# Performance work log

Hardware: AMD Instinct MI355X
Metric: run time of the kernel (lower is better)

The kernel has to match this reference:

```python
import jax, jax.numpy as jnp
import numpy as np

ROPE_BASE = 1024.0
EPS = 1e-6

def _rms_norm(x):
    return x / jnp.sqrt(jnp.mean(x * x, axis=-1, keepdims=True) + EPS)

def _rotary_tables(T, head_dim):
    steps = head_dim // 4
    inv_freq = (1.0 / ROPE_BASE) ** jnp.linspace(0.0, 1.0, steps, dtype=jnp.float32)
    inv_freq = jnp.concatenate([inv_freq, jnp.zeros(steps, dtype=jnp.float32)])  # [head_dim//2]
    theta = jnp.arange(T, dtype=jnp.float32)[:, None] * inv_freq[None, :]  # [T, head_dim//2]
    return jnp.cos(theta), jnp.sin(theta)

def _apply_rotary(x, cos, sin):
    # x: [B,H,T,hd]; cos/sin: [T, hd//2]
    d = x.shape[-1] // 2
    x1, x2 = x[..., :d], x[..., d:]
    return jnp.concatenate([x1 * cos + x2 * sin, -x1 * sin + x2 * cos], axis=-1)

def setup_inputs() -> dict:
    key = jax.random.key(0)
    ks = jax.random.split(key, 5)
    B, T, C = 4, 2048, 1024
    return {
        "x": jax.random.normal(ks[0], (B, T, C), dtype=jnp.float32),
        "v1": jax.random.normal(ks[1], (B, T, C), dtype=jnp.float32),
        "qkv_weight": 0.02 * jax.random.normal(ks[2], (3, C, C), dtype=jnp.float32),
        "c_proj_w": 0.02 * jax.random.normal(ks[3], (C, C), dtype=jnp.float32),
        "c_proj_b": jnp.zeros((C,), dtype=jnp.float32),
        "lamb": jnp.full((1,), 0.5, dtype=jnp.float32),
        "attn_window": 512,
    }

def reference(x, v1, qkv_weight, c_proj_w, c_proj_b, lamb, attn_window):
    B, T, C = x.shape
    H = 16
    hd = C // H
    # fused QKV projection: qkv_weight is [3, C, C], applied as x @ W_k^T
    qkv = jnp.einsum('btc,kdc->kbtd', x, qkv_weight)  # [3,B,T,C]
    q, k, v = qkv[0], qkv[1], qkv[2]
    def to_heads(t):
        return t.reshape(B, T, H, hd).transpose(0, 2, 1, 3)  # [B,H,T,hd]
    query, key_, value = to_heads(q), to_heads(k), to_heads(v)
    v1h = to_heads(v1)
    lam = lamb[0]
    value = (1.0 - lam) * value + lam * v1h  # value-residual blend
    query = _rms_norm(query)
    key_ = _rms_norm(key_)
    cos, sin = _rotary_tables(T, hd)
    query = _apply_rotary(query, cos, sin)
    key_ = _apply_rotary(key_, cos, sin)
    # windowed causal mask: attend iff 0 <= i - j < attn_window
    i = jnp.arange(T)[:, None]
    j = jnp.arange(T)[None, :]
    allowed = (i - j < attn_window) & (j <= i)
    bias = jnp.where(allowed, 0.0, -jnp.inf).astype(x.dtype)  # [T,T]
    scale = 1.0 / jnp.sqrt(jnp.asarray(hd, dtype=x.dtype))
    scores = jnp.einsum('bhtd,bhsd->bhts', query, key_) * scale + bias
    attn = jax.nn.softmax(scores, axis=-1)
    out = jnp.einsum('bhts,bhsd->bhtd', attn, value)  # [B,H,T,hd]
    out = out.transpose(0, 2, 1, 3).reshape(B, T, C)
    y = out @ c_proj_w.T + c_proj_b
    return (y, value)
```

## Files before the change

### kernel.cpp

```cpp
#include <hip/hip_runtime.h>
#include <stdint.h>

typedef __attribute__((ext_vector_type(8))) short short8;
typedef __attribute__((ext_vector_type(4))) float f32x4;

#define LDS_AS __attribute__((address_space(3)))
#define GLOB_AS __attribute__((address_space(1)))

__device__ __forceinline__ void gload_lds16(const void* g, void* l) {
    __builtin_amdgcn_global_load_lds((const GLOB_AS uint32_t*)g,
                                     (LDS_AS uint32_t*)l, 16, 0, 0);
}

__device__ __forceinline__ unsigned short f2bf(float f) {
    uint32_t u = __builtin_bit_cast(uint32_t, f);
    u += 0x7fffu + ((u >> 16) & 1u);
    return (unsigned short)(u >> 16);
}
__device__ __forceinline__ float bf2f(unsigned short u) {
    uint32_t v = ((uint32_t)u) << 16;
    return __builtin_bit_cast(float, v);
}

__global__ void cvt3_kernel(const float* __restrict__ s0,
                            const float* __restrict__ s1,
                            const float* __restrict__ s2,
                            unsigned short* __restrict__ d0,
                            unsigned short* __restrict__ d1,
                            unsigned short* __restrict__ d2) {
    long e = ((long)blockIdx.x * blockDim.x + threadIdx.x) * 4;
    const float* s; unsigned short* d; long off;
    if (e < 8388608)        { s = s0; d = d0; off = e; }
    else if (e < 11534336)  { s = s1; d = d1; off = e - 8388608; }
    else                    { s = s2; d = d2; off = e - 11534336; }
    float4 v = *(const float4*)(s + off);
    ushort4 o;
    o.x = f2bf(v.x); o.y = f2bf(v.y); o.z = f2bf(v.z); o.w = f2bf(v.w);
    *(ushort4*)(d + off) = o;
}

__global__ void rope_tables(float* __restrict__ cosT, float* __restrict__ sinT) {
    int tid = blockIdx.x * blockDim.x + threadIdx.x;
    int t = tid >> 5, i = tid & 31;
    float f = (i < 16) ? exp2f(-10.0f * (float)i / 15.0f) : 0.0f;
    float th = (float)t * f;
    cosT[tid] = cosf(th);
    sinT[tid] = sinf(th);
}

template <int MODE>
__global__ __launch_bounds__(512, 2) void gemm8p(
    const unsigned short* __restrict__ A, const unsigned short* __restrict__ B,
    int K,
    unsigned short* __restrict__ qbuf, unsigned short* __restrict__ kbuf,
    float* __restrict__ vout, unsigned short* __restrict__ vbT,
    const float* __restrict__ v1, const float* __restrict__ lambp,
    float* __restrict__ y, const float* __restrict__ bias,
    const float* __restrict__ cosT, const float* __restrict__ sinT)
{
    __shared__ __align__(16) char smem[147456];
    char* const AL = smem;
    char* const BL = smem + 98304;
    const int tid = threadIdx.x, lane = tid & 63, w = tid >> 6;
    const int wr = w >> 1, wc = w & 1;
    const int lr = lane & 15, lh = lane >> 4;

    const int id = blockIdx.x;
    const long m0 = (long)((id & 7) * 4 + ((id >> 3) & 3)) * 256;
    const long n0 = (long)(id >> 5) * 128;
    const int NT = K >> 6;

    const int srow = tid >> 3;
    const int swc  = (tid & 7) ^ (srow & 7);
    const long rsb = (long)K * 2;
    const char* pa0 = (const char*)A + (m0 + srow +   0) * rsb + swc * 16;
    const char* pa1 = (const char*)A + (m0 + srow +  64) * rsb + swc * 16;
    const char* pa2 = (const char*)A + (m0 + srow + 128) * rsb + swc * 16;
    const char* pa3 = (const char*)A + (m0 + srow + 192) * rsb + swc * 16;
    const char* pb0 = (const char*)B + (n0 + srow +   0) * rsb + swc * 16;
    const char* pb1 = (const char*)B + (n0 + srow +  64) * rsb + swc * 16;
    char* const lA = AL + w * 1024;
    char* const lB = BL + w * 1024;

    auto STAGE_A3 = [&](int aoff, int boff) {
        gload_lds16(pa0, lA + aoff);
        gload_lds16(pa1, lA + aoff + 8192);
        gload_lds16(pb0, lB + boff);
    };
    auto STAGE_B3 = [&](int aoff, int boff) {
        gload_lds16(pa2, lA + aoff + 16384);
        gload_lds16(pa3, lA + aoff + 24576);
        gload_lds16(pb1, lB + boff + 8192);
        pa0 += 128; pa1 += 128; pa2 += 128; pa3 += 128;
        pb0 += 128; pb1 += 128;
    };

    const int arow_b = (wr * 64 + lr) * 128;
    const int brow_b = (wc * 64 + lr) * 128;
    const int x0 = ((lh)     ^ (lr & 7)) * 16;
    const int x1 = ((4 + lh) ^ (lr & 7)) * 16;

    f32x4 acc[4][4] = {};

    STAGE_A3(0, 0);           STAGE_B3(0, 0);
    STAGE_A3(32768, 16384);   STAGE_B3(32768, 16384);

    int cA = 0, cB = 0;
    int sA = 65536, sB = 32768;

    for (int t = 0; t < NT; ++t) {
        if (t < NT - 1) asm volatile("s_waitcnt vmcnt(6)" ::: "memory");
        else            asm volatile("s_waitcnt vmcnt(0)" ::: "memory");
        __builtin_amdgcn_s_barrier();
        __builtin_amdgcn_sched_barrier(0);

        const char* ab = AL + cA;
        const char* bb = BL + cB;
        const bool st = (t < NT - 2);

        short8 bfr[4][2], afr[2][2];
        #pragma unroll
        for (int ni = 0; ni < 4; ++ni) {
            bfr[ni][0] = *(const short8*)(bb + brow_b + ni * 2048 + x0);
            bfr[ni][1] = *(const short8*)(bb + brow_b + ni * 2048 + x1);
        }
        #pragma unroll
        for (int mi = 0; mi < 2; ++mi) {
            afr[mi][0] = *(const short8*)(ab + arow_b + mi * 2048 + x0);
            afr[mi][1] = *(const short8*)(ab + arow_b + mi * 2048 + x1);
        }
        if (st) STAGE_A3(sA, sB);
        __builtin_amdgcn_s_barrier();
        asm volatile("s_waitcnt lgkmcnt(0)" ::: "memory");
        __builtin_amdgcn_sched_barrier(0);
        __builtin_amdgcn_s_setprio(1);
        #pragma unroll
        for (int mi = 0; mi < 2; ++mi)
            #pragma unroll
            for (int ni = 0; ni < 4; ++ni)
                #pragma unroll
                for (int ks = 0; ks < 2; ++ks)
                    acc[mi][ni] = __builtin_amdgcn_mfma_f32_16x16x32_bf16(
                        afr[mi][ks], bfr[ni][ks], acc[mi][ni], 0, 0, 0);
        __builtin_amdgcn_s_setprio(0);
        __builtin_amdgcn_s_barrier();

        short8 afr2[2][2];
        #pragma unroll
        for (int mi = 0; mi < 2; ++mi) {
            afr2[mi][0] = *(const short8*)(ab + arow_b + (mi + 2) * 2048 + x0);
            afr2[mi][1] = *(const short8*)(ab + arow_b + (mi + 2) * 2048 + x1);
        }
        if (st) STAGE_B3(sA, sB);
        __builtin_amdgcn_s_barrier();
        asm volatile("s_waitcnt lgkmcnt(0)" ::: "memory");
        __builtin_amdgcn_sched_barrier(0);
        __builtin_amdgcn_s_setprio(1);
        #pragma unroll
        for (int mi = 0; mi < 2; ++mi)
            #pragma unroll
            for (int ni = 0; ni < 4; ++ni)
                #pragma unroll
                for (int ks = 0; ks < 2; ++ks)
                    acc[mi + 2][ni] = __builtin_amdgcn_mfma_f32_16x16x32_bf16(
                        afr2[mi][ks], bfr[ni][ks], acc[mi + 2][ni], 0, 0, 0);
        __builtin_amdgcn_s_setprio(0);

        cA = (cA == 65536) ? 0 : cA + 32768;
        cB = (cB == 32768) ? 0 : cB + 16384;
        sA = (sA == 65536) ? 0 : sA + 32768;
        sB = (sB == 32768) ? 0 : sB + 16384;
    }

    if constexpr (MODE == 1) {
        const long nbase = n0 + wc * 64;
        const int kk = (int)(nbase >> 10);
        const int h = (int)((nbase & 1023) >> 6);
        if (kk == 2) {
            float lam = lambp[0];
            #pragma unroll
            for (int i = 0; i < 4; ++i)
            #pragma unroll
            for (int j = 0; j < 4; ++j)
            #pragma unroll
            for (int r = 0; r < 4; ++r) {
                long m = m0 + wr * 64 + i * 16 + lh * 4 + r;
                int d = j * 16 + lr;
                int rem = h * 64 + d;
                long b_ = m >> 11, t = m & 2047;
                size_t idx = (((size_t)(b_ * 16 + h)) * 2048 + t) * 64 + d;
                float vv = v1[(size_t)m * 1024 + rem];
                float val = (1.0f - lam) * acc[i][j][r] + lam * vv;
                vout[idx] = val;
                vbT[(((size_t)(b_ * 16 + h)) * 64 + d) * 2048 + t] = f2bf(val);
            }
        } else {
            unsigned short* dst = (kk == 0) ? qbuf : kbuf;
            #pragma unroll
            for (int i = 0; i < 4; ++i)
            #pragma unroll
            for (int r = 0; r < 4; ++r) {
                float v0 = acc[i][0][r], v1_ = acc[i][1][r];
                float v2 = acc[i][2][r], v3 = acc[i][3][r];
                float ss = v0 * v0 + v1_ * v1_ + v2 * v2 + v3 * v3;
                ss += __shfl_xor(ss, 1);
                ss += __shfl_xor(ss, 2);
                ss += __shfl_xor(ss, 4);
                ss += __shfl_xor(ss, 8);
                float inv = rsqrtf(ss * (1.0f / 64.0f) + 1e-6f);
                float x0f = v0 * inv, x1f = v1_ * inv;
                float x2f = v2 * inv, x3f = v3 * inv;
                long m = m0 + wr * 64 + i * 16 + lh * 4 + r;
                int t = (int)(m & 2047);
                long b_ = m >> 11;
                float c0 = cosT[t * 32 + lr],      s0 = sinT[t * 32 + lr];
                float c1 = cosT[t * 32 + 16 + lr], s1 = sinT[t * 32 + 16 + lr];
                size_t rb = (((size_t)(b_ * 16 + h)) * 2048 + t) * 64;
                dst[rb + 0 * 16 + lr] = f2bf( x0f * c0 + x2f * s0);
                dst[rb + 1 * 16 + lr] = f2bf( x1f * c1 + x3f * s1);
                dst[rb + 2 * 16 + lr] = f2bf(-x0f * s0 + x2f * c0);
                dst[rb + 3 * 16 + lr] = f2bf(-x1f * s1 + x3f * c1);
            }
        }
    } else {
        #pragma unroll
        for (int i = 0; i < 4; ++i)
        #pragma unroll
        for (int j = 0; j < 4; ++j)
        #pragma unroll
        for (int r = 0; r < 4; ++r) {
            long m = m0 + wr * 64 + i * 16 + lh * 4 + r;
            long n = n0 + wc * 64 + j * 16 + lr;
            y[(size_t)m * 1024 + n] = acc[i][j][r] + bias[n];
        }
    }
}

__global__ __launch_bounds__(512, 2) void attn_kernel(
    const unsigned short* __restrict__ qn, const unsigned short* __restrict__ kn,
    const unsigned short* __restrict__ vtb, unsigned short* __restrict__ attn_out,
    const int* __restrict__ winp)
{
    __shared__ unsigned short Ks[2][64 * 64];
    __shared__ unsigned short Vt[2][64 * 64];
    __shared__ unsigned short Pl[8][16 * 72];
    const int tid = threadIdx.x, lane = tid & 63, w = tid >> 6;
    const int lr = lane & 15, lh = lane >> 4;
    const int bh = blockIdx.x;
    const int qt2 = blockIdx.y;
    const int t0 = qt2 * 128;
    const int win = winp[0];
    const int qrow = t0 + w * 16;

    short8 qf[2];
    #pragma unroll
    for (int ks = 0; ks < 2; ++ks)
        qf[ks] = *(const short8*)&qn[((size_t)bh * 2048 + qrow + lr) * 64 + ks * 32 + lh * 8];

    const int srow = tid >> 3;
    const int scol = (tid & 7) ^ (srow & 7);
    const char* kg = (const char*)kn + ((size_t)bh * 2048 + srow) * 128 + scol * 16;
    const char* vg = (const char*)vtb + ((size_t)(bh * 64 + srow)) * 4096 + scol * 16;
    char* lk = (char*)&Ks[0][0] + w * 1024;
    char* lv = (char*)&Vt[0][0] + w * 1024;

    auto STAGE = [&](int buf, int j0) {
        gload_lds16(kg + (size_t)j0 * 128, lk + buf * 8192);
        gload_lds16(vg + (size_t)j0 * 2,   lv + buf * 8192);
    };

    f32x4 oacc[4] = {};
    float mrow[4], lrow[4];
    #pragma unroll
    for (int r = 0; r < 4; ++r) { mrow[r] = -1e30f; lrow[r] = 0.f; }

    const float C = 0.125f * 1.44269504f;
    const int kvt0 = max(0, t0 - win + 1) >> 6;
    const int kvt1 = (t0 + 127) >> 6;

    STAGE(0, kvt0 * 64);
    __syncthreads();
    for (int kvt = kvt0; kvt <= kvt1; ++kvt) {
        const int j0 = kvt * 64;
        const int buf = (kvt - kvt0) & 1;
        if (kvt < kvt1) STAGE(buf ^ 1, j0 + 64);

        if (j0 <= qrow + 15 && j0 + 63 >= qrow + 16 - win) {
            const char* ksb = (const char*)&Ks[buf][0];
            const char* vtb_ = (const char*)&Vt[buf][0];

            float sv[4][4];
            #pragma unroll
            for (int kt = 0; kt < 4; ++kt) {
                f32x4 s = {};
                #pragma unroll
                for (int ks = 0; ks < 2; ++ks) {
                    int row = kt * 16 + lr;
                    int off = row * 128 + (((ks * 4 + lh) ^ (row & 7)) * 16);
                    short8 kf = *(const short8*)(ksb + off);
                    s = __builtin_amdgcn_mfma_f32_16x16x32_bf16(qf[ks], kf, s, 0, 0, 0);
                }
                #pragma unroll
                for (int r = 0; r < 4; ++r) {
                    int qi = qrow + lh * 4 + r;
                    int ji = j0 + kt * 16 + lr;
                    bool ok = (ji <= qi) && (qi - ji < win);
                    sv[kt][r] = ok ? s[r] * C : -1e30f;
                }
            }

            float pn[4][4];
            #pragma unroll
            for (int r = 0; r < 4; ++r) {
                float tm = fmaxf(fmaxf(sv[0][r], sv[1][r]), fmaxf(sv[2][r], sv[3][r]));
                #pragma unroll
                for (int m = 1; m < 16; m <<= 1) tm = fmaxf(tm, __shfl_xor(tm, m));
                float nm = fmaxf(mrow[r], tm);
                float alpha = exp2f(mrow[r] - nm);
                float ps = 0.f;
                #pragma unroll
                for (int kt = 0; kt < 4; ++kt) {
                    float p = exp2f(sv[kt][r] - nm);
                    pn[kt][r] = p; ps += p;
                }
                #pragma unroll
                for (int m = 1; m < 16; m <<= 1) ps += __shfl_xor(ps, m);
                lrow[r] = lrow[r] * alpha + ps;
                mrow[r] = nm;
                #pragma unroll
                for (int dt = 0; dt < 4; ++dt) oacc[dt][r] *= alpha;
            }

            #pragma unroll
            for (int kt = 0; kt < 4; ++kt)
                #pragma unroll
                for (int r = 0; r < 4; ++r)
                    Pl[w][(lh * 4 + r) * 72 + kt * 16 + lr] = f2bf(pn[kt][r]);

            short8 pf[2];
            #pragma unroll
            for (int ks = 0; ks < 2; ++ks)
                pf[ks] = *(const short8*)&Pl[w][lr * 72 + ks * 32 + lh * 8];
            #pragma unroll
            for (int dt = 0; dt < 4; ++dt)
                #pragma unroll
                for (int ks = 0; ks < 2; ++ks) {
                    int row = dt * 16 + lr;
                    int off = row * 128 + (((ks * 4 + lh) ^ (row & 7)) * 16);
                    short8 vf = *(const short8*)(vtb_ + off);
                    oacc[dt] = __builtin_amdgcn_mfma_f32_16x16x32_bf16(pf[ks], vf, oacc[dt], 0, 0, 0);
                }
        }
        __syncthreads();
    }

    int b = bh >> 4, h = bh & 15;
    #pragma unroll
    for (int dt = 0; dt < 4; ++dt)
        #pragma unroll
        for (int r = 0; r < 4; ++r) {
            int t = qrow + lh * 4 + r;
            float o = oacc[dt][r] / lrow[r];
            attn_out[((size_t)b * 2048 + t) * 1024 + h * 64 + dt * 16 + lr] = f2bf(o);
        }
}

extern "C" void kernel_launch(void* const* d_in, const int* in_sizes, int n_in,
                              void* d_out, int out_size, void* d_ws, size_t ws_size,
                              hipStream_t stream) {
    const float* x    = (const float*)d_in[0];
    const float* v1   = (const float*)d_in[1];
    const float* qkvw = (const float*)d_in[2];
    const float* cpw  = (const float*)d_in[3];
    const float* cpb  = (const float*)d_in[4];
    const float* lamb = (const float*)d_in[5];
    const int*   winp = (const int*)d_in[6];

    float* y    = (float*)d_out;
    float* vout = y + (size_t)8192 * 1024;

    unsigned short* vbT = (unsigned short*)y;

    char* ws = (char*)d_ws;
    unsigned short* xb   = (unsigned short*)(ws);
    unsigned short* Wb   = (unsigned short*)(ws + (16u << 20));
    unsigned short* Wp   = (unsigned short*)(ws + (22u << 20));
    unsigned short* qbuf = (unsigned short*)(ws + (24u << 20));
    unsigned short* kbuf = (unsigned short*)(ws + (40u << 20));
    float* cosT = (float*)(ws + (56u << 20));
    float* sinT = (float*)(ws + (56u << 20) + (256u << 10));

    cvt3_kernel<<<12288, 256, 0, stream>>>(x, qkvw, cpw, xb, Wb, Wp);
    rope_tables<<<65536 / 256, 256, 0, stream>>>(cosT, sinT);

    gemm8p<1><<<768, 512, 0, stream>>>(xb, Wb, 1024,
        qbuf, kbuf, vout, vbT, v1, lamb, nullptr, nullptr, cosT, sinT);

    attn_kernel<<<dim3(64, 16), 512, 0, stream>>>(qbuf, kbuf, vbT, xb, winp);

    gemm8p<2><<<256, 512, 0, stream>>>(xb, Wp, 1024,
        nullptr, nullptr, nullptr, nullptr, nullptr, nullptr, y, cpb, nullptr, nullptr);
}
```

Before: 184.9 us.

## Triple-buffer attention KV staging and fuse rope tables into convert kernel

The attention kernel moves from a double-buffered K/V LDS pipeline with two __syncthreads per tile to a three-slot ring. It prefetches two tiles ahead and uses explicit vmcnt waits plus a single barrier per iteration, so more global loads stay in flight and the trailing barrier is gone. Separately, the rope cos/sin table computation is folded into the bf16 conversion kernel as extra blocks, removing one kernel launch. The cost is more LDS per block, which may limit occupancy, and manual waitcnt/barrier ordering that must stay correct for the wrap-around slot reuse.

```diff
diff --git a/kernel.cpp b/kernel.cpp
--- a/kernel.cpp
+++ b/kernel.cpp
@@ -22,12 +22,26 @@
     return __builtin_bit_cast(float, v);
 }
 
-__global__ void cvt3_kernel(const float* __restrict__ s0,
-                            const float* __restrict__ s1,
-                            const float* __restrict__ s2,
-                            unsigned short* __restrict__ d0,
-                            unsigned short* __restrict__ d1,
-                            unsigned short* __restrict__ d2) {
+#define WAIT_VM(N)   asm volatile("s_waitcnt vmcnt(" #N ")" ::: "memory")
+#define BAR()        asm volatile("s_barrier" ::: "memory")
+#define FENCE()      __builtin_amdgcn_sched_barrier(0)
+
+__global__ void cvt3r_kernel(const float* __restrict__ s0,
+                             const float* __restrict__ s1,
+                             const float* __restrict__ s2,
+                             unsigned short* __restrict__ d0,
+                             unsigned short* __restrict__ d1,
+                             unsigned short* __restrict__ d2,
+                             float* __restrict__ cosT, float* __restrict__ sinT) {
+    if (blockIdx.x >= 12288) {
+        int tid = (blockIdx.x - 12288) * 256 + threadIdx.x;
+        int t = tid >> 5, i = tid & 31;
+        float f = (i < 16) ? exp2f(-10.0f * (float)i / 15.0f) : 0.0f;
+        float th = (float)t * f;
+        cosT[tid] = cosf(th);
+        sinT[tid] = sinf(th);
+        return;
+    }
     long e = ((long)blockIdx.x * blockDim.x + threadIdx.x) * 4;
     const float* s; unsigned short* d; long off;
     if (e < 8388608)        { s = s0; d = d0; off = e; }
@@ -37,15 +51,6 @@
     ushort4 o;
     o.x = f2bf(v.x); o.y = f2bf(v.y); o.z = f2bf(v.z); o.w = f2bf(v.w);
     *(ushort4*)(d + off) = o;
-}
-
-__global__ void rope_tables(float* __restrict__ cosT, float* __restrict__ sinT) {
-    int tid = blockIdx.x * blockDim.x + threadIdx.x;
-    int t = tid >> 5, i = tid & 31;
-    float f = (i < 16) ? exp2f(-10.0f * (float)i / 15.0f) : 0.0f;
-    float th = (float)t * f;
-    cosT[tid] = cosf(th);
-    sinT[tid] = sinf(th);
 }
 
 template <int MODE>
@@ -241,8 +246,8 @@
     const unsigned short* __restrict__ vtb, unsigned short* __restrict__ attn_out,
     const int* __restrict__ winp)
 {
-    __shared__ unsigned short Ks[2][64 * 64];
-    __shared__ unsigned short Vt[2][64 * 64];
+    __shared__ unsigned short Ks[3][64 * 64];
+    __shared__ unsigned short Vt[3][64 * 64];
     __shared__ unsigned short Pl[8][16 * 72];
     const int tid = threadIdx.x, lane = tid & 63, w = tid >> 6;
     const int lr = lane & 15, lh = lane >> 4;
@@ -264,9 +269,9 @@
     char* lk = (char*)&Ks[0][0] + w * 1024;
     char* lv = (char*)&Vt[0][0] + w * 1024;
 
-    auto STAGE = [&](int buf, int j0) {
-        gload_lds16(kg + (size_t)j0 * 128, lk + buf * 8192);
-        gload_lds16(vg + (size_t)j0 * 2,   lv + buf * 8192);
+    auto STAGE = [&](int slot, int j0) {
+        gload_lds16(kg + (size_t)j0 * 128, lk + slot * 8192);
+        gload_lds16(vg + (size_t)j0 * 2,   lv + slot * 8192);
     };
 
     f32x4 oacc[4] = {};
@@ -279,15 +284,19 @@
     const int kvt1 = (t0 + 127) >> 6;
 
     STAGE(0, kvt0 * 64);
-    __syncthreads();
+    STAGE(1, kvt0 * 64 + 64);
     for (int kvt = kvt0; kvt <= kvt1; ++kvt) {
+        const int ti = kvt - kvt0;
         const int j0 = kvt * 64;
-        const int buf = (kvt - kvt0) & 1;
-        if (kvt < kvt1) STAGE(buf ^ 1, j0 + 64);
+        if (kvt < kvt1) WAIT_VM(2);
+        else            WAIT_VM(0);
+        BAR();
+        FENCE();
+        if (kvt + 2 <= kvt1) STAGE((ti + 2) % 3, j0 + 128);
 
         if (j0 <= qrow + 15 && j0 + 63 >= qrow + 16 - win) {
-            const char* ksb = (const char*)&Ks[buf][0];
-            const char* vtb_ = (const char*)&Vt[buf][0];
+            const char* ksb = (const char*)&Ks[ti % 3][0];
+            const char* vtb_ = (const char*)&Vt[ti % 3][0];
 
             float sv[4][4];
             #pragma unroll
@@ -351,7 +360,6 @@
                     oacc[dt] = __builtin_amdgcn_mfma_f32_16x16x32_bf16(pf[ks], vf, oacc[dt], 0, 0, 0);
                 }
         }
-        __syncthreads();
     }
 
     int b = bh >> 4, h = bh & 15;
@@ -390,8 +398,7 @@
     float* cosT = (float*)(ws + (56u << 20));
     float* sinT = (float*)(ws + (56u << 20) + (256u << 10));
 
-    cvt3_kernel<<<12288, 256, 0, stream>>>(x, qkvw, cpw, xb, Wb, Wp);
-    rope_tables<<<65536 / 256, 256, 0, stream>>>(cosT, sinT);
+    cvt3r_kernel<<<12544, 256, 0, stream>>>(x, qkvw, cpw, xb, Wb, Wp, cosT, sinT);
 
     gemm8p<1><<<768, 512, 0, stream>>>(xb, Wb, 1024,
         qbuf, kbuf, vout, vbT, v1, lamb, nullptr, nullptr, cosT, sinT);
```

Measured after the change: 189.1 us. +2.3%, slower.
